# Optimization experiments

Hardware: AMD Instinct MI355X
Metric: run time of the kernel (lower is better)

Reference implementation:

```python
import jax, jax.numpy as jnp
import numpy as np

# mxfp4 (e2m1) code table: codes 0..7 positive, 8..15 negative
FP4_TABLE = jnp.array([0.0, 0.5, 1.0, 1.5, 2.0, 3.0, 4.0, 6.0,
                       -0.0, -0.5, -1.0, -1.5, -2.0, -3.0, -4.0, -6.0], dtype=jnp.float32)
# representable fp4 levels (sorted) and decision midpoints for round-to-nearest
LEVELS = jnp.array([-6., -4., -3., -2., -1.5, -1., -0.5, 0., 0.5, 1., 1.5, 2., 3., 4., 6.], dtype=jnp.float32)
MIDS = (LEVELS[1:] + LEVELS[:-1]) * 0.5
BLOCK = 32
ALPHA = 1.702
LIMIT = 7.0


def dequant_mxfp4(codes, scales):
    """codes: [E, R, C] fp4 codes; scales: [E, R//32, C] integer exponents.
    Block-scaled dequant along the reduction dim R (blocks of 32)."""
    E, R, C = codes.shape
    w = FP4_TABLE[codes]                                   # [E, R, C]
    s = jnp.exp2(scales.astype(jnp.float32) - 12.0)        # e8m0-style power-of-two scale
    w = w.reshape(E, R // BLOCK, BLOCK, C) * s[:, :, None, :]
    return w.reshape(E, R, C)


def fake_quant_mxfp4(x):
    """mxfp4 quantize-dequantize of activations, blocks of 32 along last dim,
    with straight-through estimator so the same function serves fwd and bwd."""
    shp = x.shape
    xb = x.reshape(shp[:-1] + (shp[-1] // BLOCK, BLOCK))
    amax = jnp.max(jnp.abs(xb), axis=-1, keepdims=True)
    # largest fp4 magnitude is 6 (~2^2.58); shared exponent = floor(log2(amax)) - 2
    scale = jnp.exp2(jnp.floor(jnp.log2(jnp.maximum(amax, 1e-30))) - 2.0)
    q = LEVELS[jnp.searchsorted(MIDS, xb / scale)] * scale
    q = jnp.where(amax > 0, q, 0.0).reshape(shp)
    return x + jax.lax.stop_gradient(q - x)


def moe_forward(hidden_states, routing_indices, routing_weights,
                gate_up_codes, gate_up_scales, gate_up_bias,
                down_codes, down_scales, down_bias):
    B, H = hidden_states.shape[0], hidden_states.shape[-1]
    E = gate_up_codes.shape[0]
    x = hidden_states.reshape(-1, H)                       # [T, H]
    xq = fake_quant_mxfp4(x)
    w_gu = dequant_mxfp4(gate_up_codes, gate_up_scales)    # [E, H, 2I]
    w_dn = dequant_mxfp4(down_codes, down_scales)          # [E, I, H]
    gate_up = jnp.einsum('th,ehf->etf', xq, w_gu) + gate_up_bias[:, None, :]
    gate = jnp.minimum(gate_up[..., 0::2], LIMIT)
    up = jnp.clip(gate_up[..., 1::2], -LIMIT, LIMIT)
    gated = (up + 1.0) * (gate * jax.nn.sigmoid(gate * ALPHA))
    gq = fake_quant_mxfp4(gated)                           # activation fp4 quant before down proj
    out = jnp.einsum('eti,eih->eth', gq, w_dn) + down_bias[:, None, :]
    # combine weights: combine[e, t] = sum_k routing_weights[t, k] * (routing_indices[t, k] == e)
    onehot = (routing_indices[..., None] == jnp.arange(E)).astype(out.dtype)  # [T, K, E]
    combine = jnp.einsum('tke->et', onehot * routing_weights[..., None])
    next_states = jnp.einsum('eth,et->th', out, combine)
    return next_states.reshape(B, -1, H)


def setup_inputs() -> dict:
    key = jax.random.key(0)
    ks = jax.random.split(key, 9)
    E, H, I, T, K = 8, 2880, 2880, 1024, 4
    hidden_states = jax.random.normal(ks[0], (1, T, H), dtype=jnp.float32)
    routing_indices = jax.random.randint(ks[1], (T, K), 0, E, dtype=jnp.int32)
    rw = jax.random.uniform(ks[2], (T, K), dtype=jnp.float32)
    routing_weights = rw / jnp.sum(rw, axis=-1, keepdims=True)
    gate_up_codes = jax.random.randint(ks[3], (E, H, 2 * I), 0, 16, dtype=jnp.int32)
    gate_up_scales = jax.random.randint(ks[4], (E, H // BLOCK, 2 * I), 0, 5, dtype=jnp.int32)
    gate_up_bias = 0.02 * jax.random.normal(ks[5], (E, 2 * I), dtype=jnp.float32)
    down_codes = jax.random.randint(ks[6], (E, I, H), 0, 16, dtype=jnp.int32)
    down_scales = jax.random.randint(ks[7], (E, I // BLOCK, H), 0, 5, dtype=jnp.int32)
    down_bias = 0.02 * jax.random.normal(ks[8], (E, H), dtype=jnp.float32)
    return {'hidden_states': hidden_states, 'routing_indices': routing_indices,
            'routing_weights': routing_weights, 'gate_up_codes': gate_up_codes,
            'gate_up_scales': gate_up_scales, 'gate_up_bias': gate_up_bias,
            'down_codes': down_codes, 'down_scales': down_scales, 'down_bias': down_bias}


def reference(hidden_states, routing_indices, routing_weights,
              gate_up_codes, gate_up_scales, gate_up_bias,
              down_codes, down_scales, down_bias):
    return moe_forward(hidden_states, routing_indices, routing_weights,
                       gate_up_codes, gate_up_scales, gate_up_bias,
                       down_codes, down_scales, down_bias)
```

## Files before the change

### kernel.cpp

```cpp
#include <hip/hip_runtime.h>
#include <hip/hip_bf16.h>

typedef unsigned char u8;
typedef unsigned int u32;
typedef unsigned long long u64;
typedef int i32x4 __attribute__((ext_vector_type(4)));
typedef int i32x8 __attribute__((ext_vector_type(8)));
typedef float f32x16 __attribute__((ext_vector_type(16)));

#define HD 2880
#define GUN 5760
#define NEXP 8
#define NTOK 1024
#define NASSIGN 4096
#define MAXPAD 5120
#define MAXTILES 40
#define SROWS 90
#define RB 1440
#define XSB 120
#define APART 13312
#define BPGU 13312
#define BPDN 6656

__device__ __forceinline__ void gll16(const void* g, void* l) {
  __builtin_amdgcn_global_load_lds(
      (const __attribute__((address_space(1))) u32*)g,
      (__attribute__((address_space(3))) u32*)l, 16, 0, 0);
}

__device__ __forceinline__ i32x8 ext8(i32x4 v) {
  return __builtin_shufflevector(v, v, 0, 1, 2, 3, -1, -1, -1, -1);
}

__device__ __forceinline__ int quant_code(float v, float inv) {
  float x = v * inv;
  float a = fabsf(x);
  int n;
  if (x > 0.f)
    n = (a > 0.25f) + (a > 0.75f) + (a > 1.25f) + (a > 1.75f) +
        (a > 2.5f)  + (a > 3.5f)  + (a > 5.f);
  else
    n = (a >= 0.25f) + (a >= 0.75f) + (a >= 1.25f) + (a >= 1.75f) +
        (a >= 2.5f)  + (a >= 3.5f)  + (a >= 5.f);
  return x < 0.f ? (8 | n) : n;
}

__global__ __launch_bounds__(256)
void route_k(const int* __restrict__ ridx, const float* __restrict__ rw,
             int* __restrict__ tt_e, int* __restrict__ tt_row0, int* __restrict__ tt_rows,
             int* __restrict__ atok, int* __restrict__ tok2row) {
  __shared__ int cnt[NEXP], cur[NEXP], poff[NEXP];
  int tid = threadIdx.x;
  if (tid < NEXP) { cnt[tid] = 0; cur[tid] = 0; }
  __syncthreads();
  for (int a = tid; a < NASSIGN; a += 256) atomicAdd(&cnt[ridx[a]], 1);
  __syncthreads();
  if (tid == 0) {
    int off = 0, nt = 0;
    for (int e = 0; e < NEXP; ++e) {
      poff[e] = off;
      int cc = cnt[e];
      int ntl = (cc + 127) >> 7;
      for (int i = 0; i < ntl; ++i) {
        int rem = cc - i * 128;
        tt_e[nt] = e; tt_row0[nt] = off + i * 128; tt_rows[nt] = rem < 128 ? rem : 128;
        ++nt;
      }
      off += ntl * 128;
    }
    for (; nt < 64; ++nt) { tt_e[nt] = 0; tt_row0[nt] = 0; tt_rows[nt] = 0; }
  }
  __syncthreads();
  for (int r2 = tid; r2 < MAXPAD; r2 += 256) atok[r2] = 0;
  __syncthreads();
  for (int a = tid; a < NASSIGN; a += 256) {
    int e = ridx[a];
    int p = atomicAdd(&cur[e], 1);
    int r2 = poff[e] + p;
    atok[r2] = a >> 2;
    tok2row[a] = r2;
  }
}

__device__ __forceinline__ void quant_x_body(int t, int tid, const float* __restrict__ x,
                                             u8* __restrict__ xqp, u8* __restrict__ xs) {
  if (tid >= 360) return;
  const float* xp = x + (long)t * HD + tid * 8;
  float4 v0 = *reinterpret_cast<const float4*>(xp);
  float4 v1 = *reinterpret_cast<const float4*>(xp + 4);
  float vv[8] = {v0.x, v0.y, v0.z, v0.w, v1.x, v1.y, v1.z, v1.w};
  float am = 0.f;
#pragma unroll
  for (int j = 0; j < 8; ++j) am = fmaxf(am, fabsf(vv[j]));
  am = fmaxf(am, __shfl_xor(am, 1));
  am = fmaxf(am, __shfl_xor(am, 2));
  u32 eb = (__float_as_uint(am) >> 23) & 255u;
  float inv = __uint_as_float((256u - eb) << 23);
  u32 w = 0;
#pragma unroll
  for (int j = 0; j < 8; ++j) {
    u32 c = (am > 0.f) ? (u32)quant_code(vv[j], inv) : 0u;
    w |= c << (4 * j);
  }
  *reinterpret_cast<u32*>(xqp + (long)t * RB + tid * 4) = w;
  if ((tid & 3) == 0) {
    int kb = tid >> 2;
    int p = kb / 6, j = kb % 6;
    xs[(long)t * XSB + p * 8 + j] = (u8)(am > 0.f ? (eb - 2u) : 0u);
  }
}

__device__ __forceinline__ void repack_gu_body(int idx, int tid,
                                               const int* __restrict__ codes,
                                               const int* __restrict__ scales,
                                               u8* __restrict__ wqgT) {
  const int ND = GUN;
  const int tile = idx / 15;
  const int p = idx % 15;
  const int nt = tile % 45;
  const int e = tile / 45;
  u8* base = wqgT + ((long)tile * 15 + p) * BPGU;
#pragma unroll
  for (int i = 0; i < 2; ++i) {
    int c = tid + i * 384;
    int col = c & 127, kb = c >> 7;
    const int f = nt * 128 + col;
    const int* src = codes + ((long)e * HD + (p * 6 + kb) * 32) * ND + f;
    u32 w[4] = {0, 0, 0, 0};
#pragma unroll
    for (int j = 0; j < 32; ++j) {
      u32 cc = (u32)src[(long)j * ND] & 15u;
      w[j >> 3] |= cc << ((j & 7) * 4);
    }
    *reinterpret_cast<uint4*>(base + c * 16) = make_uint4(w[0], w[1], w[2], w[3]);
  }
  if (tid < 128) {
    const int f = nt * 128 + tid;
    u64 v = 0;
#pragma unroll
    for (int kb = 0; kb < 6; ++kb) {
      u32 s = (u32)(scales[((long)e * SROWS + p * 6 + kb) * ND + f] + 115) & 255u;
      v |= (u64)s << (kb * 8);
    }
    *reinterpret_cast<u64*>(base + 12288 + tid * 8) = v;
  }
}

__global__ __launch_bounds__(384)
void prep1_k(const float* __restrict__ x, u8* __restrict__ xqp, u8* __restrict__ xs,
             const int* __restrict__ guc, const int* __restrict__ gus,
             u8* __restrict__ wqgT) {
  const int b = blockIdx.x;
  const int tid = threadIdx.x;
  if (b < NTOK) quant_x_body(b, tid, x, xqp, xs);
  else repack_gu_body(b - NTOK, tid, guc, gus, wqgT);
}

__device__ __forceinline__ void repack_dn_body(int idx, int tid,
                                               const int* __restrict__ codes,
                                               const int* __restrict__ scales,
                                               u8* __restrict__ wqdT) {
  const int ND = HD;
  const int tile = idx / 15;
  const int p = idx % 15;
  const int nt = tile % 45;
  const int e = tile / 45;
  u8* base = wqdT + ((long)tile * 15 + p) * BPDN;
#pragma unroll
  for (int i = 0; i < 2; ++i) {
    int c = tid + i * 256;
    if (c < 384) {
      int col = c & 63, kb = c >> 6;
      const int f = nt * 64 + col;
      const int* src = codes + ((long)e * HD + (p * 6 + kb) * 32) * ND + f;
      u32 w[4] = {0, 0, 0, 0};
#pragma unroll
      for (int j = 0; j < 32; ++j) {
        u32 cc = (u32)src[(long)j * ND] & 15u;
        w[j >> 3] |= cc << ((j & 7) * 4);
      }
      *reinterpret_cast<uint4*>(base + c * 16) = make_uint4(w[0], w[1], w[2], w[3]);
    }
  }
  if (tid < 64) {
    const int f = nt * 64 + tid;
    u64 v = 0;
#pragma unroll
    for (int kb = 0; kb < 6; ++kb) {
      u32 s = (u32)(scales[((long)e * SROWS + p * 6 + kb) * ND + f] + 115) & 255u;
      v |= (u64)s << (kb * 8);
    }
    *reinterpret_cast<u64*>(base + 6144 + tid * 8) = v;
  }
}

__global__ __launch_bounds__(384)
void gathx_k(const u8* __restrict__ xqp, const u8* __restrict__ xs,
             const int* __restrict__ atok, u8* __restrict__ xqT) {
  const int mt = blockIdx.x;
  const int tid = threadIdx.x;
  __shared__ int toks[128];
  if (tid < 128) toks[tid] = atok[mt * 128 + tid];
  __syncthreads();
  u8* base = xqT + (long)mt * (15 * APART);
#pragma unroll
  for (int i = 0; i < 30; ++i) {
    int idx = tid + i * 384;
    int p = idx / 768, rem = idx % 768;
    uint4 v = *reinterpret_cast<const uint4*>(xqp + (long)toks[rem & 127] * RB +
                                              p * 96 + (rem >> 7) * 16);
    *reinterpret_cast<uint4*>(base + (long)p * APART + rem * 16) = v;
  }
#pragma unroll
  for (int i = 0; i < 5; ++i) {
    int idx = tid + i * 384;
    int p = idx >> 7, row = idx & 127;
    u64 v = *reinterpret_cast<const u64*>(xs + (long)toks[row] * XSB + p * 8);
    *reinterpret_cast<u64*>(base + (long)p * APART + 12288 + row * 8) = v;
  }
}

__device__ __forceinline__ void gu_gemm_body(
    int lin, const u8* __restrict__ xqT, const u8* __restrict__ wqgT,
    const float* __restrict__ gub,
    const int* __restrict__ tt_e, const int* __restrict__ tt_rows,
    u8* __restrict__ gqT) {
  int xcd = lin & 7, pos = lin >> 3;
  int L = xcd * 225 + pos;
  int mt = L % 40, nt = L / 40;

  const int rows = tt_rows[mt];
  if (rows <= 0) return;
  const int e = tt_e[mt];
  const int tid = threadIdx.x;
  const int lane = tid & 63;
  const int wid = tid >> 6;
  const int wm = wid & 1;
  const int wn = wid >> 1;
  const int ml = lane & 31;
  const int kc = lane >> 5;

  __shared__ __align__(16) u8 Tiles[2][26624];

  const u8* Abase = xqT + (long)mt * (15 * APART);
  const u8* Bbase = wqgT + (long)(e * 45 + nt) * (15 * BPGU);

  const u8* csrc[7]; int cstep[7], cdst[7]; bool cval[7];
#pragma unroll
  for (int i = 0; i < 7; ++i) {
    int c = tid + i * 256;
    cval[i] = (c < 1664);
    if (c < 832)       { csrc[i] = Abase + c * 16;         cstep[i] = APART; cdst[i] = c * 16; }
    else if (c < 1664) { csrc[i] = Bbase + (c - 832) * 16; cstep[i] = BPGU;  cdst[i] = 13312 + (c - 832) * 16; }
    else               { csrc[i] = Abase; cstep[i] = 0; cdst[i] = 0; }
  }
  auto stage = [&](int buf, int p) {
#pragma unroll
    for (int i = 0; i < 7; ++i)
      if (cval[i]) gll16(csrc[i] + (long)p * cstep[i], &Tiles[buf][cdst[i]]);
  };

  stage(0, 0);

  f32x16 acc[2][2];
#pragma unroll
  for (int a_ = 0; a_ < 2; ++a_)
#pragma unroll
    for (int b_ = 0; b_ < 2; ++b_)
#pragma unroll
      for (int k_ = 0; k_ < 16; ++k_) acc[a_][b_][k_] = 0.f;

  const int row0l = wm * 64 + ml;
  const int col0l = wn * 64 + ml;
  const bool act = (wm == 0) || (rows > 64);

  __syncthreads();

  for (int p = 0; p < 15; ++p) {
    const int cur = p & 1;
    if (p + 1 < 15) stage(cur ^ 1, p + 1);
    if (act) {
      const u8* T = Tiles[cur];
      u64 As0 = *reinterpret_cast<const u64*>(&T[12288 + row0l * 8]);
      u64 As1 = *reinterpret_cast<const u64*>(&T[12288 + (row0l + 32) * 8]);
      u64 Bs0 = *reinterpret_cast<const u64*>(&T[25600 + col0l * 8]);
      u64 Bs1 = *reinterpret_cast<const u64*>(&T[25600 + (col0l + 32) * 8]);
#pragma unroll
      for (int t = 0; t < 3; ++t) {
        const int kb = t * 2 + kc;
        const int sh = kb * 8;
        i32x4 af0 = *reinterpret_cast<const i32x4*>(&T[(kb * 128 + row0l) * 16]);
        i32x4 af1 = *reinterpret_cast<const i32x4*>(&T[(kb * 128 + row0l + 32) * 16]);
        i32x4 bf0 = *reinterpret_cast<const i32x4*>(&T[13312 + (kb * 128 + col0l) * 16]);
        i32x4 bf1 = *reinterpret_cast<const i32x4*>(&T[13312 + (kb * 128 + col0l + 32) * 16]);
        int sa0 = (int)((As0 >> sh) & 255), sa1 = (int)((As1 >> sh) & 255);
        int sb0 = (int)((Bs0 >> sh) & 255), sb1 = (int)((Bs1 >> sh) & 255);
        __builtin_amdgcn_s_setprio(1);
        acc[0][0] = __builtin_amdgcn_mfma_scale_f32_32x32x64_f8f6f4(
            ext8(af0), ext8(bf0), acc[0][0], 4, 4, 0, sa0, 0, sb0);
        acc[0][1] = __builtin_amdgcn_mfma_scale_f32_32x32x64_f8f6f4(
            ext8(af0), ext8(bf1), acc[0][1], 4, 4, 0, sa0, 0, sb1);
        acc[1][0] = __builtin_amdgcn_mfma_scale_f32_32x32x64_f8f6f4(
            ext8(af1), ext8(bf0), acc[1][0], 4, 4, 0, sa1, 0, sb0);
        acc[1][1] = __builtin_amdgcn_mfma_scale_f32_32x32x64_f8f6f4(
            ext8(af1), ext8(bf1), acc[1][1], 4, 4, 0, sa1, 0, sb1);
        __builtin_amdgcn_s_setprio(0);
      }
    }
    __syncthreads();
  }

  const int hlf = lane >> 5;
  u8* Glds = &Tiles[0][0];
  const int pdn = nt / 3;
  const int kb0 = 2 * (nt % 3);
  bool evenl = ((lane & 1) == 0);
#pragma unroll
  for (int mf = 0; mf < 2; ++mf) {
    float gated[2][16];
#pragma unroll
    for (int nf = 0; nf < 2; ++nf) {
      int fgc = nt * 128 + wn * 64 + nf * 32 + ml;
      float bown = gub[e * GUN + fgc];
#pragma unroll
      for (int rr = 0; rr < 16; ++rr) {
        float z = acc[mf][nf][rr] + bown;
        float zp = __shfl_xor(z, 1);
        float g = evenl ? z : zp;
        float u = evenl ? zp : z;
        g = fminf(g, 7.f);
        u = fminf(fmaxf(u, -7.f), 7.f);
        float sg = 1.f / (1.f + expf(-1.702f * g));
        gated[nf][rr] = (u + 1.f) * (g * sg);
      }
    }
#pragma unroll
    for (int rr = 0; rr < 16; ++rr) {
      float am = fmaxf(fabsf(gated[0][rr]), fabsf(gated[1][rr]));
      am = fmaxf(am, __shfl_xor(am, 2));
      am = fmaxf(am, __shfl_xor(am, 4));
      am = fmaxf(am, __shfl_xor(am, 8));
      am = fmaxf(am, __shfl_xor(am, 16));
      u32 eb = (__float_as_uint(am) >> 23) & 255u;
      float inv = __uint_as_float((256u - eb) << 23);
      int c0 = (am > 0.f) ? quant_code(gated[0][rr], inv) : 0;
      int c1 = (am > 0.f) ? quant_code(gated[1][rr], inv) : 0;
      int b0 = c0 | (__shfl_xor(c0, 2) << 4);
      int b1 = c1 | (__shfl_xor(c1, 2) << 4);
      int mrow = (rr & 3) + 8 * (rr >> 2) + 4 * hlf;
      int rloc = wm * 64 + mf * 32 + mrow;
      if ((lane & 3) == 0) {
        Glds[rloc * 32 + wn * 16 + (ml >> 2)] = (u8)b0;
        Glds[rloc * 32 + wn * 16 + 8 + (ml >> 2)] = (u8)b1;
        if (rloc < rows && ml == 0)
          gqT[((long)mt * 15 + pdn) * APART + 12288 + rloc * 8 + kb0 + wn] =
              (u8)(am > 0.f ? (eb - 2u) : 0u);
      }
    }
  }
  __syncthreads();
  {
    int part = tid >> 7, row = tid & 127;
    uint4 v = *reinterpret_cast<const uint4*>(&Glds[row * 32 + part * 16]);
    *reinterpret_cast<uint4*>(gqT + ((long)mt * 15 + pdn) * APART +
                              ((kb0 + part) * 128 + row) * 16) = v;
  }
}

__global__ __launch_bounds__(256, 3)
void gu_fused_k(const u8* __restrict__ xqT, const u8* __restrict__ wqgT,
                const float* __restrict__ gub,
                const int* __restrict__ tt_e, const int* __restrict__ tt_rows,
                u8* __restrict__ gqT,
                const int* __restrict__ dnc, const int* __restrict__ dns,
                u8* __restrict__ wqdT) {
  if (blockIdx.x < 1800)
    gu_gemm_body(blockIdx.x, xqT, wqgT, gub, tt_e, tt_rows, gqT);
  else
    repack_dn_body(blockIdx.x - 1800, threadIdx.x, dnc, dns, wqdT);
}

__global__ __launch_bounds__(128, 2)
void dn_k(const u8* __restrict__ gqT, const u8* __restrict__ wqdT,
          const float* __restrict__ dnb,
          const int* __restrict__ tt_e, const int* __restrict__ tt_rows,
          float* __restrict__ partial) {
  int lin = blockIdx.x;
  int xcd = lin & 7, pos = lin >> 3;
  int L = xcd * 225 + pos;
  int mt = L % 40, nt = L / 40;

  const int rows = tt_rows[mt];
  if (rows <= 0) return;
  const int e = tt_e[mt];
  const int tid = threadIdx.x;
  const int lane = tid & 63;
  const int wid = tid >> 6;
  const int wm = wid;
  const int ml = lane & 31;
  const int kc = lane >> 5;

  __shared__ __align__(16) u8 Tiles[2][19968];

  const u8* Abase = gqT + (long)mt * (15 * APART);
  const u8* Bbase = wqdT + (long)(e * 45 + nt) * (15 * BPDN);

  const u8* csrc[10]; int cstep[10], cdst[10]; bool cval[10];
#pragma unroll
  for (int i = 0; i < 10; ++i) {
    int c = tid + i * 128;
    cval[i] = (c < 1248);
    if (c < 832)       { csrc[i] = Abase + c * 16;         cstep[i] = APART; cdst[i] = c * 16; }
    else if (c < 1248) { csrc[i] = Bbase + (c - 832) * 16; cstep[i] = BPDN;  cdst[i] = 13312 + (c - 832) * 16; }
    else               { csrc[i] = Abase; cstep[i] = 0; cdst[i] = 0; }
  }
  auto stage = [&](int buf, int p) {
#pragma unroll
    for (int i = 0; i < 10; ++i)
      if (cval[i]) gll16(csrc[i] + (long)p * cstep[i], &Tiles[buf][cdst[i]]);
  };

  stage(0, 0);

  f32x16 acc[2][2];
#pragma unroll
  for (int a_ = 0; a_ < 2; ++a_)
#pragma unroll
    for (int b_ = 0; b_ < 2; ++b_)
#pragma unroll
      for (int k_ = 0; k_ < 16; ++k_) acc[a_][b_][k_] = 0.f;

  const int row0l = wm * 64 + ml;
  const int col0l = ml;
  const bool act = (wm == 0) || (rows > 64);

  __syncthreads();

  for (int p = 0; p < 15; ++p) {
    const int cur = p & 1;
    if (p + 1 < 15) stage(cur ^ 1, p + 1);
    if (act) {
      const u8* T = Tiles[cur];
      u64 As0 = *reinterpret_cast<const u64*>(&T[12288 + row0l * 8]);
      u64 As1 = *reinterpret_cast<const u64*>(&T[12288 + (row0l + 32) * 8]);
      u64 Bs0 = *reinterpret_cast<const u64*>(&T[19456 + col0l * 8]);
      u64 Bs1 = *reinterpret_cast<const u64*>(&T[19456 + (col0l + 32) * 8]);
#pragma unroll
      for (int t = 0; t < 3; ++t) {
        const int kb = t * 2 + kc;
        const int sh = kb * 8;
        i32x4 af0 = *reinterpret_cast<const i32x4*>(&T[(kb * 128 + row0l) * 16]);
        i32x4 af1 = *reinterpret_cast<const i32x4*>(&T[(kb * 128 + row0l + 32) * 16]);
        i32x4 bf0 = *reinterpret_cast<const i32x4*>(&T[13312 + (kb * 64 + col0l) * 16]);
        i32x4 bf1 = *reinterpret_cast<const i32x4*>(&T[13312 + (kb * 64 + col0l + 32) * 16]);
        int sa0 = (int)((As0 >> sh) & 255), sa1 = (int)((As1 >> sh) & 255);
        int sb0 = (int)((Bs0 >> sh) & 255), sb1 = (int)((Bs1 >> sh) & 255);
        __builtin_amdgcn_s_setprio(1);
        acc[0][0] = __builtin_amdgcn_mfma_scale_f32_32x32x64_f8f6f4(
            ext8(af0), ext8(bf0), acc[0][0], 4, 4, 0, sa0, 0, sb0);
        acc[0][1] = __builtin_amdgcn_mfma_scale_f32_32x32x64_f8f6f4(
            ext8(af0), ext8(bf1), acc[0][1], 4, 4, 0, sa0, 0, sb1);
        acc[1][0] = __builtin_amdgcn_mfma_scale_f32_32x32x64_f8f6f4(
            ext8(af1), ext8(bf0), acc[1][0], 4, 4, 0, sa1, 0, sb0);
        acc[1][1] = __builtin_amdgcn_mfma_scale_f32_32x32x64_f8f6f4(
            ext8(af1), ext8(bf1), acc[1][1], 4, 4, 0, sa1, 0, sb1);
        __builtin_amdgcn_s_setprio(0);
      }
    }
    __syncthreads();
  }

  const int hlf = lane >> 5;
  const int row0 = mt * 128;
#pragma unroll
  for (int mf = 0; mf < 2; ++mf) {
#pragma unroll
    for (int rr = 0; rr < 16; ++rr) {
      int mrow = (rr & 3) + 8 * (rr >> 2) + 4 * hlf;
      int rloc = wm * 64 + mf * 32 + mrow;
      if (rloc >= rows) continue;
      long rg = row0 + rloc;
#pragma unroll
      for (int nf = 0; nf < 2; ++nf) {
        int hg = nt * 64 + nf * 32 + ml;
        partial[rg * HD + hg] = acc[mf][nf][rr] + dnb[e * HD + hg];
      }
    }
  }
}

__global__ __launch_bounds__(768)
void gather_k(const float* __restrict__ partial, const int* __restrict__ tok2row,
              const float* __restrict__ rw, float* __restrict__ out) {
  int t = blockIdx.x;
  int i = threadIdx.x;
  if (i >= 720) return;
  int c = i * 4;
  float4 s = make_float4(0.f, 0.f, 0.f, 0.f);
#pragma unroll
  for (int k = 0; k < 4; ++k) {
    int r = tok2row[t * 4 + k];
    float w = rw[t * 4 + k];
    float4 v = *reinterpret_cast<const float4*>(&partial[(long)r * HD + c]);
    s.x += w * v.x; s.y += w * v.y; s.z += w * v.z; s.w += w * v.w;
  }
  *reinterpret_cast<float4*>(&out[(long)t * HD + c]) = s;
}

extern "C" void kernel_launch(void* const* d_in, const int* in_sizes, int n_in,
                              void* d_out, int out_size, void* d_ws, size_t ws_size,
                              hipStream_t stream) {
  (void)in_sizes; (void)n_in; (void)ws_size; (void)out_size;
  const float* x   = (const float*)d_in[0];
  const int* ridx  = (const int*)d_in[1];
  const float* rw  = (const float*)d_in[2];
  const int* guc   = (const int*)d_in[3];
  const int* gus   = (const int*)d_in[4];
  const float* gub = (const float*)d_in[5];
  const int* dnc   = (const int*)d_in[6];
  const int* dns   = (const int*)d_in[7];
  const float* dnb = (const float*)d_in[8];
  float* out = (float*)d_out;
  char* ws = (char*)d_ws;

  int* tt_e    = (int*)(ws);
  int* tt_row0 = (int*)(ws + 1024);
  int* tt_rows = (int*)(ws + 2048);
  int* atok    = (int*)(ws + 4096);
  int* tok2row = (int*)(ws + 4096 + MAXPAD * 4);
  size_t off = 65536;
  u8* xqp = (u8*)(ws + off);  off += (size_t)NTOK * RB;
  u8* xs  = (u8*)(ws + off);  off += (size_t)NTOK * XSB;
  u8* xqT = (u8*)(ws + off);  off += (size_t)MAXTILES * 15 * APART;
  u8* gqT = (u8*)(ws + off);  off += (size_t)MAXTILES * 15 * APART;
  u8* wqgT = (u8*)(ws + off); off += (size_t)NEXP * 45 * 15 * BPGU;
  u8* wqdT = (u8*)(ws + off); off += (size_t)NEXP * 45 * 15 * BPDN;
  float* partial = (float*)(ws + off); off += (size_t)MAXPAD * HD * 4;

  route_k<<<1, 256, 0, stream>>>(ridx, rw, tt_e, tt_row0, tt_rows, atok, tok2row);
  prep1_k<<<NTOK + 5400, 384, 0, stream>>>(x, xqp, xs, guc, gus, wqgT);
  gathx_k<<<MAXTILES, 384, 0, stream>>>(xqp, xs, atok, xqT);
  gu_fused_k<<<1800 + 5400, 256, 0, stream>>>(xqT, wqgT, gub, tt_e, tt_rows, gqT,
                                              dnc, dns, wqdT);
  dn_k<<<1800, 128, 0, stream>>>(gqT, wqdT, dnb, tt_e, tt_rows, partial);
  gather_k<<<NTOK, 768, 0, stream>>>(partial, tok2row, rw, out);
}
```

Measured before the change: 379.8 us.

## Fuse weighted token gather into down-proj epilogue with atomic adds

Drops the large fp32 partial buffer and the separate gather kernel. The down-projection epilogue now scales each row by its routing weight and atomically adds it into the output row of the owning token. A small zero kernel clears the output first, and route_k now records per-row weights. This removes a full write and re-read of the padded partial tensor, at the cost of roughly 12M float atomics and a summation order that is no longer deterministic.

```diff
diff --git a/kernel.cpp b/kernel.cpp
--- a/kernel.cpp
+++ b/kernel.cpp
@@ -46,9 +46,16 @@
 }
 
 __global__ __launch_bounds__(256)
+void zero_k(float4* __restrict__ p, int n4) {
+  int i = blockIdx.x * 256 + threadIdx.x;
+  int stride = gridDim.x * 256;
+  for (; i < n4; i += stride) p[i] = make_float4(0.f, 0.f, 0.f, 0.f);
+}
+
+__global__ __launch_bounds__(256)
 void route_k(const int* __restrict__ ridx, const float* __restrict__ rw,
              int* __restrict__ tt_e, int* __restrict__ tt_row0, int* __restrict__ tt_rows,
-             int* __restrict__ atok, int* __restrict__ tok2row) {
+             int* __restrict__ atok, float* __restrict__ awt) {
   __shared__ int cnt[NEXP], cur[NEXP], poff[NEXP];
   int tid = threadIdx.x;
   if (tid < NEXP) { cnt[tid] = 0; cur[tid] = 0; }
@@ -71,14 +78,14 @@
     for (; nt < 64; ++nt) { tt_e[nt] = 0; tt_row0[nt] = 0; tt_rows[nt] = 0; }
   }
   __syncthreads();
-  for (int r2 = tid; r2 < MAXPAD; r2 += 256) atok[r2] = 0;
+  for (int r2 = tid; r2 < MAXPAD; r2 += 256) { atok[r2] = 0; awt[r2] = 0.f; }
   __syncthreads();
   for (int a = tid; a < NASSIGN; a += 256) {
     int e = ridx[a];
     int p = atomicAdd(&cur[e], 1);
     int r2 = poff[e] + p;
     atok[r2] = a >> 2;
-    tok2row[a] = r2;
+    awt[r2] = rw[a];
   }
 }
 
@@ -384,7 +391,8 @@
 void dn_k(const u8* __restrict__ gqT, const u8* __restrict__ wqdT,
           const float* __restrict__ dnb,
           const int* __restrict__ tt_e, const int* __restrict__ tt_rows,
-          float* __restrict__ partial) {
+          const int* __restrict__ atok, const float* __restrict__ awt,
+          float* __restrict__ out) {
   int lin = blockIdx.x;
   int xcd = lin & 7, pos = lin >> 3;
   int L = xcd * 225 + pos;
@@ -480,37 +488,22 @@
       int rloc = wm * 64 + mf * 32 + mrow;
       if (rloc >= rows) continue;
       long rg = row0 + rloc;
+      float wgt = awt[rg];
+      long tok = atok[rg];
 #pragma unroll
       for (int nf = 0; nf < 2; ++nf) {
         int hg = nt * 64 + nf * 32 + ml;
-        partial[rg * HD + hg] = acc[mf][nf][rr] + dnb[e * HD + hg];
-      }
-    }
-  }
-}
-
-__global__ __launch_bounds__(768)
-void gather_k(const float* __restrict__ partial, const int* __restrict__ tok2row,
-              const float* __restrict__ rw, float* __restrict__ out) {
-  int t = blockIdx.x;
-  int i = threadIdx.x;
-  if (i >= 720) return;
-  int c = i * 4;
-  float4 s = make_float4(0.f, 0.f, 0.f, 0.f);
-#pragma unroll
-  for (int k = 0; k < 4; ++k) {
-    int r = tok2row[t * 4 + k];
-    float w = rw[t * 4 + k];
-    float4 v = *reinterpret_cast<const float4*>(&partial[(long)r * HD + c]);
-    s.x += w * v.x; s.y += w * v.y; s.z += w * v.z; s.w += w * v.w;
-  }
-  *reinterpret_cast<float4*>(&out[(long)t * HD + c]) = s;
+        float v = (acc[mf][nf][rr] + dnb[e * HD + hg]) * wgt;
+        atomicAdd(&out[tok * HD + hg], v);
+      }
+    }
+  }
 }
 
 extern "C" void kernel_launch(void* const* d_in, const int* in_sizes, int n_in,
                               void* d_out, int out_size, void* d_ws, size_t ws_size,
                               hipStream_t stream) {
-  (void)in_sizes; (void)n_in; (void)ws_size; (void)out_size;
+  (void)in_sizes; (void)n_in; (void)ws_size;
   const float* x   = (const float*)d_in[0];
   const int* ridx  = (const int*)d_in[1];
   const float* rw  = (const float*)d_in[2];
@@ -527,7 +520,7 @@
   int* tt_row0 = (int*)(ws + 1024);
   int* tt_rows = (int*)(ws + 2048);
   int* atok    = (int*)(ws + 4096);
-  int* tok2row = (int*)(ws + 4096 + MAXPAD * 4);
+  float* awt   = (float*)(ws + 4096 + MAXPAD * 4);
   size_t off = 65536;
   u8* xqp = (u8*)(ws + off);  off += (size_t)NTOK * RB;
   u8* xs  = (u8*)(ws + off);  off += (size_t)NTOK * XSB;
@@ -535,13 +528,12 @@
   u8* gqT = (u8*)(ws + off);  off += (size_t)MAXTILES * 15 * APART;
   u8* wqgT = (u8*)(ws + off); off += (size_t)NEXP * 45 * 15 * BPGU;
   u8* wqdT = (u8*)(ws + off); off += (size_t)NEXP * 45 * 15 * BPDN;
-  float* partial = (float*)(ws + off); off += (size_t)MAXPAD * HD * 4;
-
-  route_k<<<1, 256, 0, stream>>>(ridx, rw, tt_e, tt_row0, tt_rows, atok, tok2row);
+
+  zero_k<<<720, 256, 0, stream>>>((float4*)out, out_size / 4);
+  route_k<<<1, 256, 0, stream>>>(ridx, rw, tt_e, tt_row0, tt_rows, atok, awt);
   prep1_k<<<NTOK + 5400, 384, 0, stream>>>(x, xqp, xs, guc, gus, wqgT);
   gathx_k<<<MAXTILES, 384, 0, stream>>>(xqp, xs, atok, xqT);
   gu_fused_k<<<1800 + 5400, 256, 0, stream>>>(xqT, wqgT, gub, tt_e, tt_rows, gqT,
                                               dnc, dns, wqdT);
-  dn_k<<<1800, 128, 0, stream>>>(gqT, wqdT, dnb, tt_e, tt_rows, partial);
-  gather_k<<<NTOK, 768, 0, stream>>>(partial, tok2row, rw, out);
-}
+  dn_k<<<1800, 128, 0, stream>>>(gqT, wqdT, dnb, tt_e, tt_rows, atok, awt, out);
+}
```

Result: slower. 417.7 us (+10.0%).
